# Performance work log

Hardware: AMD Instinct MI355X
Metric: run time of the kernel (lower is better)

## Reference

```python
import jax, jax.numpy as jnp
import numpy as np
import math

D = 128  # hidden_dim
N_USERS = 10000
N_ITEMS = 12000
NEG_INF = -9e15


def setup_inputs() -> dict:
    key = jax.random.key(0)
    k1, k2, k3, k4, k5 = jax.random.split(key, 5)
    ufea = jax.random.normal(k1, (N_USERS, D), dtype=jnp.float32)
    inter = jax.random.normal(k2, (N_ITEMS, D), dtype=jnp.float32)
    adj = jax.random.randint(k3, (N_USERS, N_ITEMS), 0, 2, dtype=jnp.int32)
    # linear layer params (torch default init approximated with scaled normals)
    W = jax.random.normal(k4, (D, D), dtype=jnp.float32) / jnp.sqrt(jnp.float32(D))
    b = jax.random.normal(k5, (D,), dtype=jnp.float32) * 0.01
    return {"ufea": ufea, "inter": inter, "adj": adj, "W": W, "b": b}


def _leaky_relu2(x):
    # nn.LeakyReLU(2): negative_slope = 2
    return jnp.where(x > 0, x, 2.0 * x)


def reference(ufea, inter, adj, W, b):
    # GAT.forward_user with dropout in eval mode (identity).
    # Attention.forward(a=ufea, b=inter, adj)
    query = ufea @ W.T + b                      # [N, D]  nn.Linear
    scale = 1.0 / math.sqrt(D)
    scores = _leaky_relu2((query @ inter.T) * scale)   # [N, M]
    scores = jnp.where(adj > 0, scores, NEG_INF)        # mask non-edges
    attn = jax.nn.softmax(scores, axis=1)               # row softmax
    result = attn @ inter                                # [N, D]
    return result
```

## Files before the change

kernel.cpp:

```cpp
#include <hip/hip_runtime.h>
#include <cstdint>
#include <cstddef>


#define N_USERS 10000
#define N_ITEMS 12000
#define HD      128
#define QROWS   10112
#define NCHUNK  16
#define TILE    64
#define NTILES  188
#define UBLOCKS 79
#define QBLOCKS 158
#define KT_PITCH 12032

typedef __bf16 bf16x8 __attribute__((ext_vector_type(8)));
typedef __bf16 bf16x4 __attribute__((ext_vector_type(4)));
typedef __bf16 bf16x2 __attribute__((ext_vector_type(2)));
typedef float  f32x4  __attribute__((ext_vector_type(4)));
typedef int    i32x4  __attribute__((ext_vector_type(4)));

typedef const __attribute__((address_space(1))) unsigned int g_u32;
typedef __attribute__((address_space(3))) unsigned int l_u32;

__global__ __launch_bounds__(256) void cast_inter_kernel(const float* __restrict__ inter,
                                                         __bf16* __restrict__ kg,
                                                         __bf16* __restrict__ ktg) {
    __shared__ __bf16 Tl[128 * 72];
    const int t  = threadIdx.x;
    const int i0 = blockIdx.x * 64;
    for (int it = 0; it < 8; ++it) {
        int g   = it * 256 + t;
        int row = g >> 5;
        int d   = (g & 31) * 4;
        int item = i0 + row;
        if (item < N_ITEMS) {
            f32x4 v = *(const f32x4*)(inter + (size_t)item * HD + d);
            __bf16 b0 = (__bf16)v.x, b1 = (__bf16)v.y, b2 = (__bf16)v.z, b3 = (__bf16)v.w;
            bf16x4 pk = {b0, b1, b2, b3};
            *(bf16x4*)(kg + (size_t)item * HD + d) = pk;
            Tl[(d + 0) * 72 + row] = b0;
            Tl[(d + 1) * 72 + row] = b1;
            Tl[(d + 2) * 72 + row] = b2;
            Tl[(d + 3) * 72 + row] = b3;
        } else {
            Tl[(d + 0) * 72 + row] = (__bf16)0.f;
            Tl[(d + 1) * 72 + row] = (__bf16)0.f;
            Tl[(d + 2) * 72 + row] = (__bf16)0.f;
            Tl[(d + 3) * 72 + row] = (__bf16)0.f;
        }
    }
    __syncthreads();
    const int d  = t >> 1;
    const int jb = (t & 1) * 32;
    #pragma unroll
    for (int k = 0; k < 4; ++k) {
        bf16x8 v = *(const bf16x8*)&Tl[d * 72 + jb + k * 8];
        *(bf16x8*)(ktg + (size_t)d * KT_PITCH + i0 + jb + k * 8) = v;
    }
}

__global__ __launch_bounds__(256) void query_kernel(const float* __restrict__ ufea,
                                                    const float* __restrict__ W,
                                                    const float* __restrict__ bias,
                                                    __bf16* __restrict__ qg) {
    const int lane = threadIdx.x & 63, wave = threadIdx.x >> 6;
    const int n = lane & 15, qd = lane >> 4;
    const int user0 = blockIdx.x * 64 + wave * 16;
    int arow = user0 + n; if (arow > N_USERS - 1) arow = N_USERS - 1;

    bf16x8 af[4];
    #pragma unroll
    for (int kk = 0; kk < 4; ++kk) {
        const float* p = ufea + (size_t)arow * HD + kk * 32 + qd * 8;
        f32x4 lo = *(const f32x4*)p, hi = *(const f32x4*)(p + 4);
        bf16x8 a;
        a[0]=(__bf16)lo.x; a[1]=(__bf16)lo.y; a[2]=(__bf16)lo.z; a[3]=(__bf16)lo.w;
        a[4]=(__bf16)hi.x; a[5]=(__bf16)hi.y; a[6]=(__bf16)hi.z; a[7]=(__bf16)hi.w;
        af[kk] = a;
    }
    #pragma unroll
    for (int nt = 0; nt < 8; ++nt) {
        f32x4 acc = {0.f, 0.f, 0.f, 0.f};
        #pragma unroll
        for (int kk = 0; kk < 4; ++kk) {
            const float* p = W + (size_t)(nt * 16 + n) * HD + kk * 32 + qd * 8;
            f32x4 lo = *(const f32x4*)p, hi = *(const f32x4*)(p + 4);
            bf16x8 b;
            b[0]=(__bf16)lo.x; b[1]=(__bf16)lo.y; b[2]=(__bf16)lo.z; b[3]=(__bf16)lo.w;
            b[4]=(__bf16)hi.x; b[5]=(__bf16)hi.y; b[6]=(__bf16)hi.z; b[7]=(__bf16)hi.w;
            acc = __builtin_amdgcn_mfma_f32_16x16x32_bf16(af[kk], b, acc, 0, 0, 0);
        }
        const float bv = bias[nt * 16 + n];
        #pragma unroll
        for (int r = 0; r < 4; ++r) {
            int row = user0 + qd * 4 + r;
            qg[(size_t)row * HD + nt * 16 + n] = (__bf16)(acc[r] + bv);
        }
    }
}

__global__ __launch_bounds__(256, 2) void fused_kernel(const __bf16* __restrict__ qg,
                                                       const __bf16* __restrict__ kg,
                                                       const __bf16* __restrict__ ktg,
                                                       const int* __restrict__ adj,
                                                       float* __restrict__ Opart,
                                                       float* __restrict__ lpart) {
    __shared__ __bf16 Kbuf[16 * 512];
    __shared__ __bf16 Vbuf[16 * 512];
    __shared__ __bf16 Pl[4][32 * 72];
    const int lane = threadIdx.x & 63, wave = threadIdx.x >> 6;
    const int n = lane & 15, qd = lane >> 4;
    const int user0 = blockIdx.y * 128 + wave * 32;
    const int chunk = blockIdx.x;
    const int t0 = (chunk * NTILES) / NCHUNK;
    const int t1 = ((chunk + 1) * NTILES) / NCHUNK;
    const float SC = (float)(1.4426950408889634 * 0.08838834764831845);

    bf16x8 qf[2][4];
    #pragma unroll
    for (int g = 0; g < 2; ++g)
        #pragma unroll
        for (int kk = 0; kk < 4; ++kk)
            qf[g][kk] = *(const bf16x8*)(qg + (size_t)(user0 + g * 16 + n) * HD + kk * 32 + qd * 8);

    f32x4 Oacc[2][8];
    #pragma unroll
    for (int g = 0; g < 2; ++g)
        #pragma unroll
        for (int dt = 0; dt < 8; ++dt) Oacc[g][dt] = (f32x4){0.f, 0.f, 0.f, 0.f};
    float lacc[2][4] = {{0.f,0.f,0.f,0.f},{0.f,0.f,0.f,0.f}};

    int adjOff[2][4];
    #pragma unroll
    for (int g = 0; g < 2; ++g)
        #pragma unroll
        for (int r = 0; r < 4; ++r) {
            int u = user0 + g * 16 + qd * 4 + r;
            if (u > N_USERS - 1) u = N_USERS - 1;
            adjOff[g][r] = u * N_ITEMS;
        }
    __bf16* pw = &Pl[wave][0];

    for (int t = t0; t < t1; ++t) {
        const int j0 = t * TILE;
        __syncthreads();

        #pragma unroll
        for (int j = 0; j < 4; ++j) {
            const int c = wave * 4 + j;
            int row = j0 + 4 * n + wave;
            if (row > N_ITEMS - 1) row = N_ITEMS - 1;
            const __bf16* src = kg + (size_t)row * HD + j * 32 + qd * 8;
            __builtin_amdgcn_global_load_lds((g_u32*)src, (l_u32*)(&Kbuf[c * 512]), 16, 0, 0);
        }
        #pragma unroll
        for (int j = 0; j < 4; ++j) {
            const int c = wave * 4 + j;
            const int dt = c >> 1, kc = c & 1;
            const __bf16* src = ktg + (size_t)(dt * 16 + n) * KT_PITCH + j0 + kc * 32 + qd * 8;
            __builtin_amdgcn_global_load_lds((g_u32*)src, (l_u32*)(&Vbuf[c * 512]), 16, 0, 0);
        }
        i32x4 av[2][4];
        {
            int col4 = j0 + 4 * n;
            if (col4 > N_ITEMS - 4) col4 = N_ITEMS - 4;
            #pragma unroll
            for (int g = 0; g < 2; ++g)
                #pragma unroll
                for (int r = 0; r < 4; ++r)
                    av[g][r] = __builtin_nontemporal_load((const i32x4*)(adj + adjOff[g][r] + col4));
        }
        __syncthreads();

        f32x4 S[2][4];
        #pragma unroll
        for (int g = 0; g < 2; ++g)
            #pragma unroll
            for (int nt = 0; nt < 4; ++nt) S[g][nt] = (f32x4){0.f, 0.f, 0.f, 0.f};
        #pragma unroll
        for (int nt = 0; nt < 4; ++nt) {
            #pragma unroll
            for (int kk = 0; kk < 4; ++kk) {
                bf16x8 b = *(const bf16x8*)(&Kbuf[(nt * 4 + kk) * 512 + lane * 8]);
                S[0][nt] = __builtin_amdgcn_mfma_f32_16x16x32_bf16(qf[0][kk], b, S[0][nt], 0, 0, 0);
                S[1][nt] = __builtin_amdgcn_mfma_f32_16x16x32_bf16(qf[1][kk], b, S[1][nt], 0, 0, 0);
            }
        }
        #pragma unroll
        for (int g = 0; g < 2; ++g) {
            #pragma unroll
            for (int r = 0; r < 4; ++r) {
                bf16x4 pk;
                #pragma unroll
                for (int nt = 0; nt < 4; ++nt) {
                    float s = S[g][nt][r] * SC;
                    s = fminf(s, s + s);
                    const bool on = (j0 + 4 * n + nt < N_ITEMS) && (av[g][r][nt] > 0);
                    float p = on ? __builtin_amdgcn_exp2f(s) : 0.f;
                    lacc[g][r] += p;
                    pk[nt] = (__bf16)p;
                }
                *(bf16x4*)(pw + (g * 16 + qd * 4 + r) * 72 + 4 * n) = pk;
            }
        }
        #pragma unroll
        for (int kc = 0; kc < 2; ++kc) {
            bf16x8 af0 = *(const bf16x8*)(pw + (0 * 16 + n) * 72 + kc * 32 + qd * 8);
            bf16x8 af1 = *(const bf16x8*)(pw + (1 * 16 + n) * 72 + kc * 32 + qd * 8);
            #pragma unroll
            for (int dt = 0; dt < 8; ++dt) {
                bf16x8 b = *(const bf16x8*)(&Vbuf[(dt * 2 + kc) * 512 + lane * 8]);
                Oacc[0][dt] = __builtin_amdgcn_mfma_f32_16x16x32_bf16(af0, b, Oacc[0][dt], 0, 0, 0);
                Oacc[1][dt] = __builtin_amdgcn_mfma_f32_16x16x32_bf16(af1, b, Oacc[1][dt], 0, 0, 0);
            }
        }
    }

    #pragma unroll
    for (int g = 0; g < 2; ++g)
        #pragma unroll
        for (int r = 0; r < 4; ++r) {
            float v = lacc[g][r];
            v += __shfl_xor(v, 1);
            v += __shfl_xor(v, 2);
            v += __shfl_xor(v, 4);
            v += __shfl_xor(v, 8);
            lacc[g][r] = v;
        }
    const size_t cb = (size_t)chunk * QROWS;
    #pragma unroll
    for (int g = 0; g < 2; ++g)
        #pragma unroll
        for (int r = 0; r < 4; ++r) {
            const int user = user0 + g * 16 + qd * 4 + r;
            if (user < N_USERS) {
                #pragma unroll
                for (int dt = 0; dt < 8; ++dt)
                    Opart[(cb + user) * HD + dt * 16 + n] = Oacc[g][dt][r];
                if (n == 0) lpart[cb + user] = lacc[g][r];
            }
        }
}

__global__ __launch_bounds__(256) void combine_kernel(const float* __restrict__ Opart,
                                                      const float* __restrict__ lpart,
                                                      float* __restrict__ out) {
    const int g = blockIdx.x * 256 + threadIdx.x;
    const int base = g * 4;
    const int user = base >> 7;
    const int d = base & 127;
    f32x4 acc = {0.f, 0.f, 0.f, 0.f};
    float l = 0.f;
    #pragma unroll
    for (int c = 0; c < NCHUNK; ++c) {
        acc += *(const f32x4*)(Opart + ((size_t)c * QROWS + user) * HD + d);
        l += lpart[(size_t)c * QROWS + user];
    }
    if (user < N_USERS) {
        f32x4 res = acc / l;
        *(f32x4*)(out + (size_t)user * HD + d) = res;
    }
}

extern "C" void kernel_launch(void* const* d_in, const int* in_sizes, int n_in,
                              void* d_out, int out_size, void* d_ws, size_t ws_size,
                              hipStream_t stream) {
    const float* ufea = (const float*)d_in[0];
    const float* inter = (const float*)d_in[1];
    const int*   adj  = (const int*)d_in[2];
    const float* W    = (const float*)d_in[3];
    const float* bias = (const float*)d_in[4];
    float* out = (float*)d_out;

    char* ws = (char*)d_ws;
    __bf16* qg   = (__bf16*)(ws);
    __bf16* kg   = (__bf16*)(ws + 2588672);
    __bf16* ktg  = (__bf16*)(ws + 5660672);
    float*  Opart = (float*)(ws + 8740864);
    float*  lpart = (float*)(ws + 91578368);

    cast_inter_kernel<<<dim3(188), dim3(256), 0, stream>>>(inter, kg, ktg);
    query_kernel<<<dim3(QBLOCKS), dim3(256), 0, stream>>>(ufea, W, bias, qg);
    fused_kernel<<<dim3(NCHUNK, UBLOCKS), dim3(256), 0, stream>>>(qg, kg, ktg, adj, Opart, lpart);
    combine_kernel<<<dim3(1264), dim3(256), 0, stream>>>(Opart, lpart, out);
}
```

Measured before the change: 684.7 us.

## Pre-tile K/V into fragment-ordered blocks, prefetch adjacency one tile ahead

```diff
diff --git a/kernel.cpp b/kernel.cpp
--- a/kernel.cpp
+++ b/kernel.cpp
@@ -11,12 +11,10 @@
 #define TILE    64
 #define NTILES  188
 #define UBLOCKS 79
-#define QBLOCKS 158
-#define KT_PITCH 12032
+#define QBLOCKS 632
 
 typedef __bf16 bf16x8 __attribute__((ext_vector_type(8)));
 typedef __bf16 bf16x4 __attribute__((ext_vector_type(4)));
-typedef __bf16 bf16x2 __attribute__((ext_vector_type(2)));
 typedef float  f32x4  __attribute__((ext_vector_type(4)));
 typedef int    i32x4  __attribute__((ext_vector_type(4)));
 
@@ -24,11 +22,11 @@
 typedef __attribute__((address_space(3))) unsigned int l_u32;
 
 __global__ __launch_bounds__(256) void cast_inter_kernel(const float* __restrict__ inter,
-                                                         __bf16* __restrict__ kg,
-                                                         __bf16* __restrict__ ktg) {
+                                                         __bf16* __restrict__ kvg) {
     __shared__ __bf16 Tl[128 * 72];
     const int t  = threadIdx.x;
-    const int i0 = blockIdx.x * 64;
+    const int tile = blockIdx.x;
+    const int i0 = tile * 64;
     for (int it = 0; it < 8; ++it) {
         int g   = it * 256 + t;
         int row = g >> 5;
@@ -36,13 +34,10 @@
         int item = i0 + row;
         if (item < N_ITEMS) {
             f32x4 v = *(const f32x4*)(inter + (size_t)item * HD + d);
-            __bf16 b0 = (__bf16)v.x, b1 = (__bf16)v.y, b2 = (__bf16)v.z, b3 = (__bf16)v.w;
-            bf16x4 pk = {b0, b1, b2, b3};
-            *(bf16x4*)(kg + (size_t)item * HD + d) = pk;
-            Tl[(d + 0) * 72 + row] = b0;
-            Tl[(d + 1) * 72 + row] = b1;
-            Tl[(d + 2) * 72 + row] = b2;
-            Tl[(d + 3) * 72 + row] = b3;
+            Tl[(d + 0) * 72 + row] = (__bf16)v.x;
+            Tl[(d + 1) * 72 + row] = (__bf16)v.y;
+            Tl[(d + 2) * 72 + row] = (__bf16)v.z;
+            Tl[(d + 3) * 72 + row] = (__bf16)v.w;
         } else {
             Tl[(d + 0) * 72 + row] = (__bf16)0.f;
             Tl[(d + 1) * 72 + row] = (__bf16)0.f;
@@ -51,12 +46,31 @@
         }
     }
     __syncthreads();
-    const int d  = t >> 1;
-    const int jb = (t & 1) * 32;
-    #pragma unroll
-    for (int k = 0; k < 4; ++k) {
-        bf16x8 v = *(const bf16x8*)&Tl[d * 72 + jb + k * 8];
-        *(bf16x8*)(ktg + (size_t)d * KT_PITCH + i0 + jb + k * 8) = v;
+    const int lane = t & 63, wave = t >> 6;
+    const int n = lane & 15, qd = lane >> 4;
+    __bf16* tbase = kvg + (size_t)tile * (32 * 512);
+    #pragma unroll
+    for (int j = 0; j < 4; ++j) {
+        const int c = wave * 4 + j;
+        int row = i0 + 4 * n + wave;
+        bf16x8 o;
+        if (row < N_ITEMS) {
+            const float* p = inter + (size_t)row * HD + j * 32 + qd * 8;
+            f32x4 lo = *(const f32x4*)p, hi = *(const f32x4*)(p + 4);
+            o[0]=(__bf16)lo.x; o[1]=(__bf16)lo.y; o[2]=(__bf16)lo.z; o[3]=(__bf16)lo.w;
+            o[4]=(__bf16)hi.x; o[5]=(__bf16)hi.y; o[6]=(__bf16)hi.z; o[7]=(__bf16)hi.w;
+        } else {
+            #pragma unroll
+            for (int e = 0; e < 8; ++e) o[e] = (__bf16)0.f;
+        }
+        *(bf16x8*)(tbase + (size_t)c * 512 + lane * 8) = o;
+    }
+    #pragma unroll
+    for (int j = 0; j < 4; ++j) {
+        const int cc = wave * 4 + j;
+        const int dt = cc >> 1, kc = cc & 1;
+        bf16x8 v = *(const bf16x8*)&Tl[(dt * 16 + n) * 72 + kc * 32 + qd * 8];
+        *(bf16x8*)(tbase + (size_t)(16 + cc) * 512 + lane * 8) = v;
     }
 }
 
@@ -66,7 +80,7 @@
                                                     __bf16* __restrict__ qg) {
     const int lane = threadIdx.x & 63, wave = threadIdx.x >> 6;
     const int n = lane & 15, qd = lane >> 4;
-    const int user0 = blockIdx.x * 64 + wave * 16;
+    const int user0 = blockIdx.x * 16;
     int arow = user0 + n; if (arow > N_USERS - 1) arow = N_USERS - 1;
 
     bf16x8 af[4];
@@ -80,7 +94,8 @@
         af[kk] = a;
     }
     #pragma unroll
-    for (int nt = 0; nt < 8; ++nt) {
+    for (int h = 0; h < 2; ++h) {
+        const int nt = wave * 2 + h;
         f32x4 acc = {0.f, 0.f, 0.f, 0.f};
         #pragma unroll
         for (int kk = 0; kk < 4; ++kk) {
@@ -101,8 +116,7 @@
 }
 
 __global__ __launch_bounds__(256, 2) void fused_kernel(const __bf16* __restrict__ qg,
-                                                       const __bf16* __restrict__ kg,
-                                                       const __bf16* __restrict__ ktg,
+                                                       const __bf16* __restrict__ kvg,
                                                        const int* __restrict__ adj,
                                                        float* __restrict__ Opart,
                                                        float* __restrict__ lpart) {
@@ -142,36 +156,45 @@
         }
     __bf16* pw = &Pl[wave][0];
 
-    for (int t = t0; t < t1; ++t) {
-        const int j0 = t * TILE;
+    i32x4 avA[2][4], avB[2][4];
+    {
+        int col4 = t0 * TILE + 4 * n;
+        if (col4 > N_ITEMS - 4) col4 = N_ITEMS - 4;
+        #pragma unroll
+        for (int g = 0; g < 2; ++g)
+            #pragma unroll
+            for (int r = 0; r < 4; ++r)
+                avA[g][r] = __builtin_nontemporal_load((const i32x4*)(adj + adjOff[g][r] + col4));
+    }
+
+    auto tile_iter = [&](int T, i32x4 (&avu)[2][4], i32x4 (&avp)[2][4]) {
+        const int j0 = T * TILE;
         __syncthreads();
 
         #pragma unroll
         for (int j = 0; j < 4; ++j) {
             const int c = wave * 4 + j;
-            int row = j0 + 4 * n + wave;
-            if (row > N_ITEMS - 1) row = N_ITEMS - 1;
-            const __bf16* src = kg + (size_t)row * HD + j * 32 + qd * 8;
+            const __bf16* src = kvg + ((size_t)T * 32 + c) * 512 + lane * 8;
             __builtin_amdgcn_global_load_lds((g_u32*)src, (l_u32*)(&Kbuf[c * 512]), 16, 0, 0);
         }
         #pragma unroll
         for (int j = 0; j < 4; ++j) {
             const int c = wave * 4 + j;
-            const int dt = c >> 1, kc = c & 1;
-            const __bf16* src = ktg + (size_t)(dt * 16 + n) * KT_PITCH + j0 + kc * 32 + qd * 8;
+            const __bf16* src = kvg + ((size_t)T * 32 + 16 + c) * 512 + lane * 8;
             __builtin_amdgcn_global_load_lds((g_u32*)src, (l_u32*)(&Vbuf[c * 512]), 16, 0, 0);
         }
-        i32x4 av[2][4];
+        __syncthreads();
+
         {
-            int col4 = j0 + 4 * n;
+            int tn = T + 1; if (tn > t1 - 1) tn = t1 - 1;
+            int col4 = tn * TILE + 4 * n;
             if (col4 > N_ITEMS - 4) col4 = N_ITEMS - 4;
             #pragma unroll
             for (int g = 0; g < 2; ++g)
                 #pragma unroll
                 for (int r = 0; r < 4; ++r)
-                    av[g][r] = __builtin_nontemporal_load((const i32x4*)(adj + adjOff[g][r] + col4));
-        }
-        __syncthreads();
+                    avp[g][r] = __builtin_nontemporal_load((const i32x4*)(adj + adjOff[g][r] + col4));
+        }
 
         f32x4 S[2][4];
         #pragma unroll
@@ -196,7 +219,7 @@
                 for (int nt = 0; nt < 4; ++nt) {
                     float s = S[g][nt][r] * SC;
                     s = fminf(s, s + s);
-                    const bool on = (j0 + 4 * n + nt < N_ITEMS) && (av[g][r][nt] > 0);
+                    const bool on = (j0 + 4 * n + nt < N_ITEMS) && (avu[g][r][nt] > 0);
                     float p = on ? __builtin_amdgcn_exp2f(s) : 0.f;
                     lacc[g][r] += p;
                     pk[nt] = (__bf16)p;
@@ -215,6 +238,12 @@
                 Oacc[1][dt] = __builtin_amdgcn_mfma_f32_16x16x32_bf16(af1, b, Oacc[1][dt], 0, 0, 0);
             }
         }
+    };
+
+    int t = t0;
+    while (true) {
+        tile_iter(t, avA, avB); ++t; if (t >= t1) break;
+        tile_iter(t, avB, avA); ++t; if (t >= t1) break;
     }
 
     #pragma unroll
@@ -274,14 +303,13 @@
     float* out = (float*)d_out;
 
     char* ws = (char*)d_ws;
-    __bf16* qg   = (__bf16*)(ws);
-    __bf16* kg   = (__bf16*)(ws + 2588672);
-    __bf16* ktg  = (__bf16*)(ws + 5660672);
-    float*  Opart = (float*)(ws + 8740864);
-    float*  lpart = (float*)(ws + 91578368);
-
-    cast_inter_kernel<<<dim3(188), dim3(256), 0, stream>>>(inter, kg, ktg);
+    __bf16* kvg  = (__bf16*)(ws);
+    __bf16* qg   = (__bf16*)(ws + 6160384);
+    float*  Opart = (float*)(ws + 8749056);
+    float*  lpart = (float*)(ws + 91586560);
+
+    cast_inter_kernel<<<dim3(NTILES), dim3(256), 0, stream>>>(inter, kvg);
     query_kernel<<<dim3(QBLOCKS), dim3(256), 0, stream>>>(ufea, W, bias, qg);
-    fused_kernel<<<dim3(NCHUNK, UBLOCKS), dim3(256), 0, stream>>>(qg, kg, ktg, adj, Opart, lpart);
+    fused_kernel<<<dim3(NCHUNK, UBLOCKS), dim3(256), 0, stream>>>(qg, kvg, adj, Opart, lpart);
     combine_kernel<<<dim3(1264), dim3(256), 0, stream>>>(Opart, lpart, out);
 }
```

Measured after the change: 689.9 us. About the same (+0.8%).
